# Optimization experiments

Hardware: AMD Instinct MI355X
Metric: run time of the kernel (lower is better)

Reference implementation:

```python
import jax, jax.numpy as jnp
import numpy as np

# (l, C_l, C_l_TP, C_l_angular) per non-empty l-block of the filter type
FILTER_REPS = [(0, 144, 144, 1), (1, 272, 272, 1), (2, 208, 208, 1), (3, 80, 80, 1), (4, 16, 16, 1)]
FILTER_C = 720      # sum of C_l
FILTER_DIM = 2704   # sum of C_l*(2l+1)
ANG_DIM = 25        # sum of C_l_angular*(2l+1)
DIM_OUT = 52
DIM_IN = 52
Q_OUT, Q_IN, NUM_P = 16, 16, 125
SCALAR_BASIS = 12


def setup_inputs() -> dict:
    key = jax.random.key(0)
    k1, k2, k3, k4, k5 = jax.random.split(key, 5)
    N = Q_OUT * Q_IN * NUM_P
    scalar_kernel_tensor = jax.random.normal(k1, (Q_OUT, Q_IN, NUM_P, SCALAR_BASIS), dtype=jnp.float32)
    angular_kernel_tensor = jax.random.normal(k2, (N, ANG_DIM), dtype=jnp.float32)
    weights = jax.random.normal(k3, (SCALAR_BASIS, FILTER_C), dtype=jnp.float32)
    # TP mixing matrix is a constant sparse buffer (Wigner-3j based); model as sparsified dense
    dense = jax.random.normal(k4, (DIM_OUT * DIM_IN, FILTER_DIM), dtype=jnp.float32)
    mask = jax.random.uniform(k5, (DIM_OUT * DIM_IN, FILTER_DIM)) < 0.05
    TP_mixing = dense * mask.astype(jnp.float32)
    return {"scalar_kernel_tensor": scalar_kernel_tensor,
            "angular_kernel_tensor": angular_kernel_tensor,
            "weights": weights,
            "TP_mixing": TP_mixing}


def mul_scalar_angular(sc, ang):
    # sc: (N, FILTER_C), ang: (N, ANG_DIM) -> (N, FILTER_DIM)
    N = sc.shape[0]
    outs = []
    s = 0
    a = 0
    for (l, C_l, C_l_TP, C_l_ang) in FILTER_REPS:
        m = 2 * l + 1
        dim_ang = C_l_ang * m
        x = (sc[:, s:s + C_l].reshape(N, C_l_ang, C_l_TP, 1)
             * ang[:, a:a + dim_ang].reshape(N, C_l_ang, 1, m))
        outs.append(x.reshape(N, C_l * m))
        s += C_l
        a += dim_ang
    return jnp.concatenate(outs, axis=-1)


def reference(scalar_kernel_tensor, angular_kernel_tensor, weights, TP_mixing):
    N = Q_OUT * Q_IN * NUM_P
    sk = scalar_kernel_tensor.reshape(N, SCALAR_BASIS)
    # combine scalar basis with weights: (N, FILTER_C)
    sc = jnp.einsum('ns,sc->nc', sk, weights / jnp.sqrt(jnp.float32(SCALAR_BASIS)))
    # ragged segment-wise broadcast multiply: (N, FILTER_DIM)
    filt = mul_scalar_angular(sc, angular_kernel_tensor)
    # kernel = (TP_mixing @ filt.T).T == filt @ TP_mixing.T : (N, DIM_OUT*DIM_IN)
    k = filt @ TP_mixing.T
    return k.reshape(Q_OUT, Q_IN, NUM_P, DIM_OUT, DIM_IN)
```

## Files before the change

kernel.cpp:

```cpp
#include <hip/hip_runtime.h>
#include <hip/hip_bf16.h>

#define N_ROWS 32000
#define SB     12
#define FC     720
#define FD     2704
#define OCOLS  2704
#define OPAD   2816
#define ANGD   25
#define PDIM   300
#define KST    320
#define NT     5
#define KP     2720
#define NTV    85
#define GPR    (KP/8)

#define NB_CVT 3740
#define NB_G   425
#define NBV    110
#define NB_X   5000

typedef __attribute__((ext_vector_type(8))) short bf16x8;
typedef __attribute__((ext_vector_type(4))) float f32x4;

__device__ __forceinline__ void gload16(const void* g, void* l) {
    __builtin_amdgcn_global_load_lds(
        (const __attribute__((address_space(1))) void*)g,
        (__attribute__((address_space(3))) void*)l, 16, 0, 0);
}

__device__ __forceinline__ void decode_f(int f, int& c, int& j, int& a) {
    if (f < 144)       { c = f;                         j = 0;            a = 0;  }
    else if (f < 960)  { int t = f - 144;  c = 144 + t/3; j = t - (t/3)*3; a = 1;  }
    else if (f < 2000) { int t = f - 960;  c = 416 + t/5; j = t - (t/5)*5; a = 4;  }
    else if (f < 2560) { int t = f - 2000; c = 624 + t/7; j = t - (t/7)*7; a = 9;  }
    else               { int t = f - 2560; c = 704 + t/9; j = t - (t/9)*9; a = 16; }
}

__global__ __launch_bounds__(256) void prep1(
    const float* __restrict__ TP,
    const float* __restrict__ W,
    __hip_bfloat16* __restrict__ TPb,
    __hip_bfloat16* __restrict__ Gt)
{
    const int b = blockIdx.x;
    if (b < NB_CVT) {
        const int g = b * 256 + threadIdx.x;
        if (g >= OPAD * GPR) return;
        const int o = g / GPR;
        const int k = (g - o * GPR) * 8;
        alignas(16) __hip_bfloat16 tmp[8];
        if (o < OCOLS && k + 8 <= FD) {
            const float4* p = (const float4*)(TP + (size_t)o * FD + k);
            float4 x0 = p[0], x1 = p[1];
            tmp[0] = __float2bfloat16(x0.x); tmp[1] = __float2bfloat16(x0.y);
            tmp[2] = __float2bfloat16(x0.z); tmp[3] = __float2bfloat16(x0.w);
            tmp[4] = __float2bfloat16(x1.x); tmp[5] = __float2bfloat16(x1.y);
            tmp[6] = __float2bfloat16(x1.z); tmp[7] = __float2bfloat16(x1.w);
        } else {
            #pragma unroll
            for (int u = 0; u < 8; ++u) {
                float v = (o < OCOLS && k + u < FD) ? TP[(size_t)o * FD + k + u] : 0.f;
                tmp[u] = __float2bfloat16(v);
            }
        }
        *(bf16x8*)(TPb + (size_t)o * KP + k) = *(const bf16x8*)tmp;
    } else {
        const int g = (b - NB_CVT) * 256 + threadIdx.x;
        if (g >= KST * GPR) return;
        const int p  = g / GPR;
        const int f0 = (g - p * GPR) * 8;
        const int s     = p / ANGD;
        const int alpha = p - s * ANGD;
        const float inv = 0.28867513459481288f;
        alignas(16) __hip_bfloat16 tmp[8];
        #pragma unroll
        for (int u = 0; u < 8; ++u) {
            const int f = f0 + u;
            float v = 0.f;
            if (p < PDIM && f < FD) {
                int c, j, a;
                decode_f(f, c, j, a);
                if (alpha == a + j) v = W[s * FC + c] * inv;
            }
            tmp[u] = __float2bfloat16(v);
        }
        *(bf16x8*)(Gt + (size_t)p * KP + f0) = *(const bf16x8*)tmp;
    }
}

__global__ __launch_bounds__(256, 4) void fused_V_X(
    const __hip_bfloat16* __restrict__ A,
    const __hip_bfloat16* __restrict__ B,
    __hip_bfloat16* __restrict__ V,
    const float* __restrict__ sk,
    const float* __restrict__ ang,
    __hip_bfloat16* __restrict__ X)
{
    __shared__ __align__(1024) char lds[24576];

    if (blockIdx.x >= NBV) {
        const int idx = (blockIdx.x - NBV) * 256 + threadIdx.x;
        if (idx >= N_ROWS * (KST / 8)) return;
        const int n  = idx / (KST / 8);
        const int p0 = (idx - n * (KST / 8)) * 8;
        const float* skn  = sk  + (size_t)n * SB;
        const float* angn = ang + (size_t)n * ANGD;
        alignas(16) __hip_bfloat16 tmp[8];
        #pragma unroll
        for (int u = 0; u < 8; ++u) {
            const int p = p0 + u;
            float v = 0.f;
            if (p < PDIM) {
                const int s = p / ANGD;
                const int a = p - s * ANGD;
                v = skn[s] * angn[a];
            }
            tmp[u] = __float2bfloat16(v);
        }
        *(bf16x8*)(X + (size_t)n * KST + p0) = *(const bf16x8*)tmp;
        return;
    }

    char* const bufA = lds;
    char* const bufB = lds + 16384;

    const int tid  = threadIdx.x;
    const int wave = tid >> 6;
    const int lane = tid & 63;

    const int id = blockIdx.x;
    const int bn = id % 5;
    const int bm = id / 5;
    const size_t arow0 = (size_t)bm * 128;
    const size_t brow0 = (size_t)bn * 64;

    const int wr = wave >> 1;
    const int wc = wave & 1;

    const int lrow2 = lane >> 2;
    const int sslot = (((lane & 3) ^ (lrow2 & 3) ^ ((lane >> 4) & 3))) << 4;

    auto STAGE = [&](int t, int half) {
        char* const la = bufA + half * 8192;
        char* const lb = bufB + half * 4096;
        const char* ga = (const char*)A
            + (arow0 + (size_t)(wave * 16 + lrow2)) * (KP * 2)
            + (size_t)t * 64 + sslot;
        gload16(ga,                         la + wave * 1024);
        gload16(ga + (size_t)64 * (KP * 2), la + 4096 + wave * 1024);
        const char* gb = (const char*)B
            + (brow0 + (size_t)(wave * 16 + lrow2)) * (KP * 2)
            + (size_t)t * 64 + sslot;
        gload16(gb, lb + wave * 1024);
    };

    const int rl   = lane & 15;
    const int koct = lane >> 4;
    const int rslot = ((koct ^ (rl & 3) ^ ((rl >> 2) & 3))) << 4;

    STAGE(0, 0);
    STAGE(1, 1);
    asm volatile("s_waitcnt vmcnt(3)" ::: "memory");
    __builtin_amdgcn_s_barrier();

    f32x4 acc[4][2] = {};

    for (int t = 0; t < NTV; ++t) {
        char* const aC = bufA + (t & 1) * 8192;
        char* const bC = bufB + (t & 1) * 4096;

        bf16x8 af[4], bfr[2];
        #pragma unroll
        for (int m = 0; m < 4; ++m) {
            const int r = wr * 64 + m * 16 + rl;
            af[m] = *(const bf16x8*)(aC + r * 64 + rslot);
        }
        #pragma unroll
        for (int n = 0; n < 2; ++n) {
            const int r = wc * 32 + n * 16 + rl;
            bfr[n] = *(const bf16x8*)(bC + r * 64 + rslot);
        }
        asm volatile("s_waitcnt lgkmcnt(0)" ::: "memory");
        __builtin_amdgcn_sched_barrier(0);
        __builtin_amdgcn_s_barrier();

        if (t + 2 < NTV) STAGE(t + 2, t & 1);

        __builtin_amdgcn_s_setprio(1);
        #pragma unroll
        for (int m = 0; m < 4; ++m)
            #pragma unroll
            for (int n = 0; n < 2; ++n)
                acc[m][n] = __builtin_amdgcn_mfma_f32_16x16x32_bf16(
                    bfr[n], af[m], acc[m][n], 0, 0, 0);
        __builtin_amdgcn_s_setprio(0);
        __builtin_amdgcn_sched_barrier(0);

        if (t < NTV - 2)       asm volatile("s_waitcnt vmcnt(3)" ::: "memory");
        else if (t == NTV - 2) asm volatile("s_waitcnt vmcnt(0)" ::: "memory");
        if (t < NTV - 1) __builtin_amdgcn_s_barrier();
    }

    const int obase = (int)arow0 + wr * 64 + rl;
    const int pbase = (int)brow0 + wc * 32 + koct * 4;
    #pragma unroll
    for (int m = 0; m < 4; ++m) {
        const int orow = obase + m * 16;
        #pragma unroll
        for (int n = 0; n < 2; ++n) {
            const int p = pbase + n * 16;
            alignas(8) __hip_bfloat16 t4[4];
            t4[0] = __float2bfloat16(acc[m][n][0]);
            t4[1] = __float2bfloat16(acc[m][n][1]);
            t4[2] = __float2bfloat16(acc[m][n][2]);
            t4[3] = __float2bfloat16(acc[m][n][3]);
            *(uint2*)(V + (size_t)orow * KST + p) = *(const uint2*)t4;
        }
    }
}

__global__ __launch_bounds__(512, 4) void gemm_bt(
    const __hip_bfloat16* __restrict__ A,
    const __hip_bfloat16* __restrict__ B,
    float* __restrict__ C)
{
    __shared__ __align__(1024) char lds[65536];
    char* const bufA = lds;
    char* const bufB = lds + 32768;
    float* const s_c = (float*)lds;

    const int tid  = threadIdx.x;
    const int wave = tid >> 6;
    const int lane = tid & 63;

    const int bn = blockIdx.x;
    const int bm = blockIdx.y;
    const size_t arow0 = (size_t)bm * 128;
    const size_t brow0 = (size_t)bn * 128;

    const int wr = wave >> 2;
    const int wc = wave & 3;

    const int lrow  = lane >> 3;
    const int lslot = ((lane & 7) ^ (lrow & 7)) << 4;

    auto STAGE = [&](const char* gbase, size_t growbase, int t, char* lbase) {
        const char* g0 = gbase + (growbase + (size_t)(wave * 8 + lrow)) * (KST * 2)
                               + (size_t)t * 128 + lslot;
        gload16(g0,                          lbase + wave * 1024);
        gload16(g0 + (size_t)64 * (KST * 2), lbase + 8192 + wave * 1024);
    };

    const int rl   = lane & 15;
    const int koct = lane >> 4;
    const int sK0 = ((0 * 4 + koct) ^ (lane & 7)) << 4;
    const int sK1 = ((1 * 4 + koct) ^ (lane & 7)) << 4;

    STAGE((const char*)A, arow0, 0, bufA + 0);
    STAGE((const char*)B, brow0, 0, bufB + 0);
    STAGE((const char*)A, arow0, 1, bufA + 16384);
    STAGE((const char*)B, brow0, 1, bufB + 16384);
    asm volatile("s_waitcnt vmcnt(4)" ::: "memory");
    __builtin_amdgcn_s_barrier();

    f32x4 acc[4][2] = {};

    for (int t = 0; t < NT; ++t) {
        char* const aC = bufA + (t & 1) * 16384;
        char* const bC = bufB + (t & 1) * 16384;

        bf16x8 af[4][2], bfr[2][2];
        #pragma unroll
        for (int m = 0; m < 4; ++m) {
            const int r = wr * 64 + m * 16 + rl;
            af[m][0] = *(const bf16x8*)(aC + r * 128 + sK0);
            af[m][1] = *(const bf16x8*)(aC + r * 128 + sK1);
        }
        #pragma unroll
        for (int n = 0; n < 2; ++n) {
            const int r = wc * 32 + n * 16 + rl;
            bfr[n][0] = *(const bf16x8*)(bC + r * 128 + sK0);
            bfr[n][1] = *(const bf16x8*)(bC + r * 128 + sK1);
        }
        asm volatile("s_waitcnt lgkmcnt(0)" ::: "memory");
        __builtin_amdgcn_sched_barrier(0);
        __builtin_amdgcn_s_barrier();

        if (t + 2 < NT) {
            STAGE((const char*)A, arow0, t + 2, aC);
            STAGE((const char*)B, brow0, t + 2, bC);
        }

        __builtin_amdgcn_s_setprio(1);
        #pragma unroll
        for (int ks = 0; ks < 2; ++ks)
            #pragma unroll
            for (int m = 0; m < 4; ++m)
                #pragma unroll
                for (int n = 0; n < 2; ++n)
                    acc[m][n] = __builtin_amdgcn_mfma_f32_16x16x32_bf16(
                        bfr[n][ks], af[m][ks], acc[m][n], 0, 0, 0);
        __builtin_amdgcn_s_setprio(0);
        __builtin_amdgcn_sched_barrier(0);

        if (t < NT - 2)       asm volatile("s_waitcnt vmcnt(4)" ::: "memory");
        else if (t == NT - 2) asm volatile("s_waitcnt vmcnt(0)" ::: "memory");
        if (t < NT - 1) __builtin_amdgcn_s_barrier();
    }

    #pragma unroll
    for (int h = 0; h < 2; ++h) {
        __syncthreads();
        if (wr == h) {
            #pragma unroll
            for (int m = 0; m < 4; ++m) {
                const int row_l = m * 16 + rl;
                #pragma unroll
                for (int n = 0; n < 2; ++n) {
                    const int col = wc * 32 + n * 16 + koct * 4;
                    *(f32x4*)&s_c[row_l * 132 + col] = acc[m][n];
                }
            }
        }
        __syncthreads();
        #pragma unroll
        for (int rr = 0; rr < 4; ++rr) {
            const int idx  = rr * 512 + tid;
            const int row  = idx >> 5;
            const int g4   = (idx & 31) * 4;
            if ((int)brow0 + g4 < OCOLS) {
                const f32x4 v = *(const f32x4*)&s_c[row * 132 + g4];
                __builtin_nontemporal_store(v,
                    (f32x4*)(C + (size_t)(arow0 + h * 64 + row) * OCOLS + brow0 + g4));
            }
        }
    }
}

extern "C" void kernel_launch(void* const* d_in, const int* in_sizes, int n_in,
                              void* d_out, int out_size, void* d_ws, size_t ws_size,
                              hipStream_t stream)
{
    const float* sk  = (const float*)d_in[0];
    const float* ang = (const float*)d_in[1];
    const float* W   = (const float*)d_in[2];
    const float* TP  = (const float*)d_in[3];
    float* out = (float*)d_out;

    __hip_bfloat16* X   = (__hip_bfloat16*)d_ws;
    __hip_bfloat16* Vb  = X   + (size_t)N_ROWS * KST;
    __hip_bfloat16* TPb = Vb  + (size_t)OPAD * KST;
    __hip_bfloat16* Gt  = TPb + (size_t)OPAD * KP;

    prep1<<<NB_CVT + NB_G, 256, 0, stream>>>(TP, W, TPb, Gt);

    fused_V_X<<<NBV + NB_X, 256, 0, stream>>>(TPb, Gt, Vb, sk, ang, X);

    dim3 grid(OPAD / 128, N_ROWS / 128);
    gemm_bt<<<grid, 512, 0, stream>>>(X, Vb, out);
}
```

Baseline: 129.5 us.

## Fuse TP fp32-to-bf16 conversion into V GEMM A-tile loading

Removes the separate pass that converted the whole TP_mixing matrix to a padded bf16 buffer. The V GEMM now reads fp32 TP rows straight into registers, converts them to bf16, and writes them to the swizzled LDS buffer after the MFMA step. The B operand still uses direct global-to-LDS loads. This saves a full write and re-read of the bf16 copy, but the A loads now go through registers with a software prefetch, which raises register pressure and doubles the bytes fetched per tile.

```diff
diff --git a/kernel.cpp b/kernel.cpp
--- a/kernel.cpp
+++ b/kernel.cpp
@@ -15,7 +15,6 @@
 #define NTV    85
 #define GPR    (KP/8)
 
-#define NB_CVT 3740
 #define NB_G   425
 #define NBV    110
 #define NB_X   5000
@@ -37,60 +36,34 @@
     else               { int t = f - 2560; c = 704 + t/9; j = t - (t/9)*9; a = 16; }
 }
 
-__global__ __launch_bounds__(256) void prep1(
-    const float* __restrict__ TP,
+__global__ __launch_bounds__(256) void prepG(
     const float* __restrict__ W,
-    __hip_bfloat16* __restrict__ TPb,
     __hip_bfloat16* __restrict__ Gt)
 {
-    const int b = blockIdx.x;
-    if (b < NB_CVT) {
-        const int g = b * 256 + threadIdx.x;
-        if (g >= OPAD * GPR) return;
-        const int o = g / GPR;
-        const int k = (g - o * GPR) * 8;
-        alignas(16) __hip_bfloat16 tmp[8];
-        if (o < OCOLS && k + 8 <= FD) {
-            const float4* p = (const float4*)(TP + (size_t)o * FD + k);
-            float4 x0 = p[0], x1 = p[1];
-            tmp[0] = __float2bfloat16(x0.x); tmp[1] = __float2bfloat16(x0.y);
-            tmp[2] = __float2bfloat16(x0.z); tmp[3] = __float2bfloat16(x0.w);
-            tmp[4] = __float2bfloat16(x1.x); tmp[5] = __float2bfloat16(x1.y);
-            tmp[6] = __float2bfloat16(x1.z); tmp[7] = __float2bfloat16(x1.w);
-        } else {
-            #pragma unroll
-            for (int u = 0; u < 8; ++u) {
-                float v = (o < OCOLS && k + u < FD) ? TP[(size_t)o * FD + k + u] : 0.f;
-                tmp[u] = __float2bfloat16(v);
-            }
-        }
-        *(bf16x8*)(TPb + (size_t)o * KP + k) = *(const bf16x8*)tmp;
-    } else {
-        const int g = (b - NB_CVT) * 256 + threadIdx.x;
-        if (g >= KST * GPR) return;
-        const int p  = g / GPR;
-        const int f0 = (g - p * GPR) * 8;
-        const int s     = p / ANGD;
-        const int alpha = p - s * ANGD;
-        const float inv = 0.28867513459481288f;
-        alignas(16) __hip_bfloat16 tmp[8];
-        #pragma unroll
-        for (int u = 0; u < 8; ++u) {
-            const int f = f0 + u;
-            float v = 0.f;
-            if (p < PDIM && f < FD) {
-                int c, j, a;
-                decode_f(f, c, j, a);
-                if (alpha == a + j) v = W[s * FC + c] * inv;
-            }
-            tmp[u] = __float2bfloat16(v);
-        }
-        *(bf16x8*)(Gt + (size_t)p * KP + f0) = *(const bf16x8*)tmp;
-    }
+    const int g = blockIdx.x * 256 + threadIdx.x;
+    if (g >= KST * GPR) return;
+    const int p  = g / GPR;
+    const int f0 = (g - p * GPR) * 8;
+    const int s     = p / ANGD;
+    const int alpha = p - s * ANGD;
+    const float inv = 0.28867513459481288f;
+    alignas(16) __hip_bfloat16 tmp[8];
+    #pragma unroll
+    for (int u = 0; u < 8; ++u) {
+        const int f = f0 + u;
+        float v = 0.f;
+        if (p < PDIM && f < FD) {
+            int c, j, a;
+            decode_f(f, c, j, a);
+            if (alpha == a + j) v = W[s * FC + c] * inv;
+        }
+        tmp[u] = __float2bfloat16(v);
+    }
+    *(bf16x8*)(Gt + (size_t)p * KP + f0) = *(const bf16x8*)tmp;
 }
 
 __global__ __launch_bounds__(256, 4) void fused_V_X(
-    const __hip_bfloat16* __restrict__ A,
+    const float* __restrict__ TP,
     const __hip_bfloat16* __restrict__ B,
     __hip_bfloat16* __restrict__ V,
     const float* __restrict__ sk,
@@ -139,16 +112,46 @@
     const int wc = wave & 1;
 
     const int lrow2 = lane >> 2;
-    const int sslot = (((lane & 3) ^ (lrow2 & 3) ^ ((lane >> 4) & 3))) << 4;
-
-    auto STAGE = [&](int t, int half) {
+    const int slog  = (lane & 3) ^ (lrow2 & 3) ^ ((lane >> 4) & 3);
+    const int sslot = slog << 4;
+
+    const int o0 = (int)arow0 + wave * 16 + lrow2;
+    const int o1 = o0 + 64;
+    const bool ok0 = o0 < OCOLS;
+    const bool ok1 = o1 < OCOLS;
+
+    float4 r00, r01, r10, r11;
+    auto A_LOAD = [&](int t) {
+        const int colf = t * 32 + slog * 8;
+        const float4 z = {0.f, 0.f, 0.f, 0.f};
+        r00 = z; r01 = z; r10 = z; r11 = z;
+        if (colf < FD) {
+            if (ok0) {
+                const float4* p = (const float4*)(TP + (size_t)o0 * FD + colf);
+                r00 = p[0]; r01 = p[1];
+            }
+            if (ok1) {
+                const float4* p = (const float4*)(TP + (size_t)o1 * FD + colf);
+                r10 = p[0]; r11 = p[1];
+            }
+        }
+    };
+    auto A_WRITE = [&](int half) {
         char* const la = bufA + half * 8192;
+        alignas(16) __hip_bfloat16 w0[8], w1[8];
+        w0[0] = __float2bfloat16(r00.x); w0[1] = __float2bfloat16(r00.y);
+        w0[2] = __float2bfloat16(r00.z); w0[3] = __float2bfloat16(r00.w);
+        w0[4] = __float2bfloat16(r01.x); w0[5] = __float2bfloat16(r01.y);
+        w0[6] = __float2bfloat16(r01.z); w0[7] = __float2bfloat16(r01.w);
+        w1[0] = __float2bfloat16(r10.x); w1[1] = __float2bfloat16(r10.y);
+        w1[2] = __float2bfloat16(r10.z); w1[3] = __float2bfloat16(r10.w);
+        w1[4] = __float2bfloat16(r11.x); w1[5] = __float2bfloat16(r11.y);
+        w1[6] = __float2bfloat16(r11.z); w1[7] = __float2bfloat16(r11.w);
+        *(bf16x8*)(la + wave * 1024 + lane * 16)        = *(const bf16x8*)w0;
+        *(bf16x8*)(la + 4096 + wave * 1024 + lane * 16) = *(const bf16x8*)w1;
+    };
+    auto B_STAGE = [&](int t, int half) {
         char* const lb = bufB + half * 4096;
-        const char* ga = (const char*)A
-            + (arow0 + (size_t)(wave * 16 + lrow2)) * (KP * 2)
-            + (size_t)t * 64 + sslot;
-        gload16(ga,                         la + wave * 1024);
-        gload16(ga + (size_t)64 * (KP * 2), la + 4096 + wave * 1024);
         const char* gb = (const char*)B
             + (brow0 + (size_t)(wave * 16 + lrow2)) * (KP * 2)
             + (size_t)t * 64 + sslot;
@@ -159,9 +162,11 @@
     const int koct = lane >> 4;
     const int rslot = ((koct ^ (rl & 3) ^ ((rl >> 2) & 3))) << 4;
 
-    STAGE(0, 0);
-    STAGE(1, 1);
-    asm volatile("s_waitcnt vmcnt(3)" ::: "memory");
+    B_STAGE(0, 0);
+    B_STAGE(1, 1);
+    A_LOAD(0); A_WRITE(0);
+    A_LOAD(1); A_WRITE(1);
+    asm volatile("s_waitcnt vmcnt(0) lgkmcnt(0)" ::: "memory");
     __builtin_amdgcn_s_barrier();
 
     f32x4 acc[4][2] = {};
@@ -185,7 +190,10 @@
         __builtin_amdgcn_sched_barrier(0);
         __builtin_amdgcn_s_barrier();
 
-        if (t + 2 < NTV) STAGE(t + 2, t & 1);
+        if (t + 2 < NTV) {
+            B_STAGE(t + 2, t & 1);
+            A_LOAD(t + 2);
+        }
 
         __builtin_amdgcn_s_setprio(1);
         #pragma unroll
@@ -197,8 +205,8 @@
         __builtin_amdgcn_s_setprio(0);
         __builtin_amdgcn_sched_barrier(0);
 
-        if (t < NTV - 2)       asm volatile("s_waitcnt vmcnt(3)" ::: "memory");
-        else if (t == NTV - 2) asm volatile("s_waitcnt vmcnt(0)" ::: "memory");
+        if (t + 2 < NTV) A_WRITE(t & 1);
+
         if (t < NTV - 1) __builtin_amdgcn_s_barrier();
     }
 
@@ -348,14 +356,13 @@
     const float* TP  = (const float*)d_in[3];
     float* out = (float*)d_out;
 
-    __hip_bfloat16* X   = (__hip_bfloat16*)d_ws;
-    __hip_bfloat16* Vb  = X   + (size_t)N_ROWS * KST;
-    __hip_bfloat16* TPb = Vb  + (size_t)OPAD * KST;
-    __hip_bfloat16* Gt  = TPb + (size_t)OPAD * KP;
-
-    prep1<<<NB_CVT + NB_G, 256, 0, stream>>>(TP, W, TPb, Gt);
-
-    fused_V_X<<<NBV + NB_X, 256, 0, stream>>>(TPb, Gt, Vb, sk, ang, X);
+    __hip_bfloat16* X  = (__hip_bfloat16*)d_ws;
+    __hip_bfloat16* Vb = X  + (size_t)N_ROWS * KST;
+    __hip_bfloat16* Gt = Vb + (size_t)OPAD * KST;
+
+    prepG<<<NB_G, 256, 0, stream>>>(W, Gt);
+
+    fused_V_X<<<NBV + NB_X, 256, 0, stream>>>(TP, Gt, Vb, sk, ang, X);
 
     dim3 grid(OPAD / 128, N_ROWS / 128);
     gemm_bt<<<grid, 512, 0, stream>>>(X, Vb, out);
```

Result: slower. 162.9 us (+25.8%).
